# Kernel optimization log

Hardware: AMD Instinct MI355X
Metric: run time of the kernel (lower is better)

Reference implementation:

```python
import jax, jax.numpy as jnp
import numpy as np
from jax import lax

D_MODEL = 1024
D_STATE = 16
D_CONV = 4
EXPAND = 2
D_INNER = EXPAND * D_MODEL          # 2048
DT_RANK = (D_MODEL + 15) // 16      # 64


def setup_inputs() -> dict:
    key = jax.random.key(0)
    ks = jax.random.split(key, 12)
    B, L = 2, 2048
    s = lambda *sh: 1.0 / np.sqrt(sh[-1])
    inp = {
        "x": jax.random.normal(ks[0], (B, L, D_MODEL), jnp.float32),
        "in_proj_w": jax.random.normal(ks[1], (2 * D_INNER, D_MODEL), jnp.float32) * s(0, D_MODEL),
        "conv_w": jax.random.normal(ks[2], (D_INNER, 1, D_CONV), jnp.float32) * s(0, D_CONV),
        "conv_b": jax.random.normal(ks[3], (D_INNER,), jnp.float32) * 0.01,
        "x_proj_w": jax.random.normal(ks[4], (DT_RANK + 2 * D_STATE, D_INNER), jnp.float32) * s(0, D_INNER),
        "dt_proj_w": jax.random.normal(ks[5], (D_INNER, DT_RANK), jnp.float32) * s(0, DT_RANK),
        "dt_proj_b": jax.random.normal(ks[6], (D_INNER,), jnp.float32) * 0.1 - 4.0,  # softplus(dt) small
        "A_log": jnp.log(jnp.broadcast_to(jnp.arange(1, D_STATE + 1, dtype=jnp.float32), (D_INNER, D_STATE))),
        "D": jnp.ones((D_INNER,), jnp.float32),
        "out_proj_w": jax.random.normal(ks[7], (D_MODEL, D_INNER), jnp.float32) * s(0, D_INNER),
        "ln_w": jnp.ones((D_MODEL,), jnp.float32),
        "ln_b": jnp.zeros((D_MODEL,), jnp.float32),
    }
    return inp


def _mamba(x, in_proj_w, conv_w, conv_b, x_proj_w, dt_proj_w, dt_proj_b, A_log, D, out_proj_w):
    B, L, _ = x.shape
    xz = jnp.einsum("bld,ed->ble", x, in_proj_w)          # [B,L,2*d_inner]
    xi, z = jnp.split(xz, 2, axis=-1)                       # each [B,L,d_inner]

    # causal depthwise conv1d over time
    xt = jnp.transpose(xi, (0, 2, 1))                       # [B,d_inner,L]
    xc = lax.conv_general_dilated(
        xt, conv_w, window_strides=(1,), padding=[(D_CONV - 1, 0)],
        dimension_numbers=("NCH", "OIH", "NCH"), feature_group_count=D_INNER)
    xc = jax.nn.silu(xc + conv_b[None, :, None])            # [B,d_inner,L]
    u = jnp.transpose(xc, (0, 2, 1))                        # [B,L,d_inner]

    x_dbl = jnp.einsum("bld,ed->ble", u, x_proj_w)          # [B,L,dt_rank+2N]
    dt, Bm, Cm = jnp.split(x_dbl, [DT_RANK, DT_RANK + D_STATE], axis=-1)
    delta = jax.nn.softplus(jnp.einsum("blr,dr->bld", dt, dt_proj_w) + dt_proj_b)  # [B,L,d_inner]

    A = -jnp.exp(A_log)                                     # [d_inner,N]

    def step(h, inputs):
        d_t, B_t, C_t, u_t = inputs                         # [B,d], [B,N], [B,N], [B,d]
        dA = jnp.exp(d_t[..., None] * A)                    # [B,d_inner,N]
        h = dA * h + (d_t * u_t)[..., None] * B_t[:, None, :]
        y_t = jnp.einsum("bdn,bn->bd", h, C_t)
        return h, y_t

    xs = (jnp.transpose(delta, (1, 0, 2)), jnp.transpose(Bm, (1, 0, 2)),
          jnp.transpose(Cm, (1, 0, 2)), jnp.transpose(u, (1, 0, 2)))
    h0 = jnp.zeros((B, D_INNER, D_STATE), x.dtype)
    _, ys = lax.scan(step, h0, xs)                          # ys [L,B,d_inner]
    y = jnp.transpose(ys, (1, 0, 2)) + u * D                # skip connection
    y = y * jax.nn.silu(z)                                  # gate
    return jnp.einsum("bld,ed->ble", y, out_proj_w)         # [B,L,d_model]


def reference(x, in_proj_w, conv_w, conv_b, x_proj_w, dt_proj_w, dt_proj_b,
              A_log, D, out_proj_w, ln_w, ln_b):
    residual = x
    y = _mamba(x, in_proj_w, conv_w, conv_b, x_proj_w, dt_proj_w, dt_proj_b,
               A_log, D, out_proj_w)
    # dropout is identity in eval; residual + LayerNorm
    h = y + residual
    mu = jnp.mean(h, axis=-1, keepdims=True)
    var = jnp.var(h, axis=-1, keepdims=True)
    return (h - mu) * lax.rsqrt(var + 1e-5) * ln_w + ln_b
```

## Files before the change

kernel.cpp:

```cpp
#include <hip/hip_runtime.h>

typedef unsigned short u16;
typedef __attribute__((ext_vector_type(8))) short bf8_t;
typedef __attribute__((ext_vector_type(4))) float f4_t;
typedef __attribute__((ext_vector_type(4))) unsigned short u16x4;
typedef __attribute__((ext_vector_type(8))) unsigned short u16x8;

__device__ __forceinline__ float b2f(u16 h) {
  union { unsigned u; float f; } v; v.u = ((unsigned)h) << 16; return v.f;
}
__device__ __forceinline__ u16 f2b(float f) {
  union { float f; unsigned u; } v; v.f = f;
  unsigned u = v.u;
  u += 0x7fffu + ((u >> 16) & 1u);
  return (u16)(u >> 16);
}

#define AS1C(p) ((const __attribute__((address_space(1))) void*)(p))
#define AS3(p)  ((__attribute__((address_space(3))) void*)(p))

__global__ __launch_bounds__(256)
void cvt_all(const float* __restrict__ x, const float* __restrict__ inW,
             const float* __restrict__ xprojW, const float* __restrict__ dtW,
             const float* __restrict__ outW,
             u16* __restrict__ xb, u16* __restrict__ inWb, u16* __restrict__ xpb,
             u16* __restrict__ dtWb, u16* __restrict__ outWb)
{
  int i = blockIdx.x * 256 + threadIdx.x;
  if (i >= 2703360) return;
  const float* s; u16* d; int off;
  if (i < 1048576)      { s = x;      d = xb;    off = i; }
  else if (i < 2097152) { s = inW;    d = inWb;  off = i - 1048576; }
  else if (i < 2146304) { s = xprojW; d = xpb;   off = i - 2097152; }
  else if (i < 2179072) { s = dtW;    d = dtWb;  off = i - 2146304; }
  else                  { s = outW;   d = outWb; off = i - 2179072; }
  f4_t v = *(const f4_t*)(s + (size_t)off * 4);
  u16x4 o;
#pragma unroll
  for (int j = 0; j < 4; ++j) o[j] = f2b(v[j]);
  *(u16x4*)(d + (size_t)off * 4) = o;
}

__device__ __forceinline__ void stage64(const u16* g, int ld, int row0, int rowmax,
                                        int k0, u16* lds, int wid, int lane) {
  int qg = (lane & 7) ^ ((lane >> 3) & 7);
#pragma unroll
  for (int c = 0; c < 4; ++c) {
    int chunk = wid * 4 + c;
    int r = row0 + chunk * 8 + (lane >> 3);
    if (r > rowmax) r = rowmax;
    const u16* gp = g + (size_t)r * ld + k0 + qg * 8;
    __builtin_amdgcn_global_load_lds(AS1C(gp), AS3(lds + chunk * 512), 16, 0, 0);
  }
}

template<int EPI>
__device__ __forceinline__ void gemm_body(const u16* __restrict__ A, int lda,
             const u16* __restrict__ Bt, int ldb,
             int Kblk, int Nact,
             u16* __restrict__ o16, float* __restrict__ of32,
             const float* __restrict__ biasf)
{
  __shared__ u16 lsA[128 * 64];
  __shared__ u16 lsB[128 * 64];
  const int tid = threadIdx.x;
  const int wid = tid >> 6, lane = tid & 63;
  const int wm = wid >> 1, wn = wid & 1;
  const int lrow = lane & 15;
  const int kq = lane >> 4;
  const int sw = lrow & 7;
  const int m0 = blockIdx.y * 128;
  const int n0 = (EPI == 1) ? 0 : blockIdx.x * 128;
  int kbase = 0;
  if (EPI == 1) kbase = blockIdx.x * Kblk;

  f4_t acc[4][4];
#pragma unroll
  for (int i = 0; i < 4; ++i)
#pragma unroll
    for (int j = 0; j < 4; ++j) acc[i][j] = {0.f, 0.f, 0.f, 0.f};

  for (int kt = kbase; kt < kbase + Kblk; kt += 64) {
    stage64(A,  lda, m0, 0x3fffffff, kt, lsA, wid, lane);
    stage64(Bt, ldb, n0, Nact - 1,   kt, lsB, wid, lane);
    __syncthreads();
#pragma unroll
    for (int h = 0; h < 2; ++h) {
      const int lk = ((h * 4 + kq) ^ sw) * 8;
      bf8_t af[4], bfr[4];
#pragma unroll
      for (int mi = 0; mi < 4; ++mi)
        af[mi] = *(const bf8_t*)&lsA[(wm * 64 + mi * 16 + lrow) * 64 + lk];
#pragma unroll
      for (int ni = 0; ni < 4; ++ni)
        bfr[ni] = *(const bf8_t*)&lsB[(wn * 64 + ni * 16 + lrow) * 64 + lk];
#pragma unroll
      for (int mi = 0; mi < 4; ++mi)
#pragma unroll
        for (int ni = 0; ni < 4; ++ni)
          acc[mi][ni] = __builtin_amdgcn_mfma_f32_16x16x32_bf16(af[mi], bfr[ni], acc[mi][ni], 0, 0, 0);
    }
    __syncthreads();
  }

  const int rq = (lane >> 4) * 4;
#pragma unroll
  for (int mi = 0; mi < 4; ++mi) {
#pragma unroll
    for (int ni = 0; ni < 4; ++ni) {
#pragma unroll
      for (int r = 0; r < 4; ++r) {
        int m = m0 + wm * 64 + mi * 16 + rq + r;
        int n = n0 + wn * 64 + ni * 16 + lrow;
        float v = acc[mi][ni][r];
        if (EPI == 1) {
          if (n < 96) of32[((size_t)blockIdx.x * 4096 + m) * 96 + n] = v;
        } else if (EPI == 2) {
          float t = v + biasf[n];
          float sp = (t > 20.f) ? t : log1pf(__expf(t));
          o16[(size_t)m * 2048 + n] = f2b(sp);
        }
      }
    }
  }
}

__global__ __launch_bounds__(256)
void gemm_xp(const u16* A, int lda, const u16* Bt, int ldb, int Kblk, int Nact,
             u16* o16, float* of32, const float* biasf)
{ gemm_body<1>(A, lda, Bt, ldb, Kblk, Nact, o16, of32, biasf); }

__global__ __launch_bounds__(256)
void gemm_dt(const u16* A, int lda, const u16* Bt, int ldb, int Kblk, int Nact,
             u16* o16, float* of32, const float* biasf)
{ gemm_body<2>(A, lda, Bt, ldb, Kblk, Nact, o16, of32, biasf); }


__device__ __forceinline__ void stageu(const u16* __restrict__ g, int ld,
                                       int row0, int k0, u16* ldsu,
                                       int wid, int lane) {
  int qg = (lane & 7) ^ ((lane >> 3) & 7);
#pragma unroll
  for (int j = 0; j < 2; ++j) {
    int rr = j * 64 + wid * 8 + (lane >> 3);
    const u16* gp = g + (size_t)(row0 + rr) * ld + k0 + qg * 8;
    __builtin_amdgcn_global_load_lds(AS1C(gp), AS3(ldsu + (j * 512 + wid * 64) * 8), 16, 0, 0);
  }
}

#define G8_BAR()   __builtin_amdgcn_s_barrier()
#define G8_LGKM0() do { asm volatile("s_waitcnt lgkmcnt(0)" ::: "memory"); \
                        __builtin_amdgcn_sched_barrier(0); } while (0)
#define G8_LGKM8() asm volatile("s_waitcnt lgkmcnt(8)" ::: "memory")
#define G8_VM(N)   do { asm volatile("s_waitcnt vmcnt(" #N ")" ::: "memory"); \
                        __builtin_amdgcn_sched_barrier(0); } while (0)

#define RD_A(base, MH) do { \
  _Pragma("unroll") \
  for (int mi_ = 0; mi_ < 4; ++mi_) { \
    af[mi_][0] = *(const bf8_t*)((base) + arow + ((MH) * 64 + mi_ * 16) * 64 + aq0); \
    af[mi_][1] = *(const bf8_t*)((base) + arow + ((MH) * 64 + mi_ * 16) * 64 + aq1); \
  } } while (0)

#define RD_B(base, NH) do { \
  _Pragma("unroll") \
  for (int ni_ = 0; ni_ < 2; ++ni_) { \
    bfr[NH][ni_][0] = *(const bf8_t*)((base) + brow + ((NH) * 32 + ni_ * 16) * 64 + aq0); \
    bfr[NH][ni_][1] = *(const bf8_t*)((base) + brow + ((NH) * 32 + ni_ * 16) * 64 + aq1); \
  } } while (0)

#define MMA(MH, NH) do { \
  __builtin_amdgcn_s_setprio(1); \
  _Pragma("unroll") \
  for (int mi_ = 0; mi_ < 4; ++mi_) \
    _Pragma("unroll") \
    for (int ni_ = 0; ni_ < 2; ++ni_) { \
      acc[(MH) * 4 + mi_][(NH) * 2 + ni_] = __builtin_amdgcn_mfma_f32_16x16x32_bf16( \
          af[mi_][0], bfr[NH][ni_][0], acc[(MH) * 4 + mi_][(NH) * 2 + ni_], 0, 0, 0); \
      acc[(MH) * 4 + mi_][(NH) * 2 + ni_] = __builtin_amdgcn_mfma_f32_16x16x32_bf16( \
          af[mi_][1], bfr[NH][ni_][1], acc[(MH) * 4 + mi_][(NH) * 2 + ni_], 0, 0, 0); \
    } \
  __builtin_amdgcn_s_setprio(0); \
} while (0)

__global__ __launch_bounds__(512, 2)
void gemm8_in(const u16* __restrict__ A, const u16* __restrict__ Bt,
              u16* __restrict__ o16)
{
  __shared__ u16 ls[65536];
  const int tid = threadIdx.x;
  const int wid = tid >> 6, lane = tid & 63;
  const int wm = wid >> 2, wn = wid & 3;
  const int lrow = lane & 15;
  const int kq = lane >> 4;
  const int sw = lrow & 7;
  const int m0 = blockIdx.y * 256;
  const int n0 = blockIdx.x * 256;
  u16* lsA0 = ls;
  u16* lsB0 = ls + 16384;
  u16* lsA1 = ls + 32768;
  u16* lsB1 = ls + 49152;
  const int arow = (wm * 128 + lrow) * 64;
  const int brow = (wn * 64 + lrow) * 64;
  const int aq0 = (kq ^ sw) * 8;
  const int aq1 = ((4 + kq) ^ sw) * 8;

  f4_t acc[8][4];
#pragma unroll
  for (int i = 0; i < 8; ++i)
#pragma unroll
    for (int j = 0; j < 4; ++j) acc[i][j] = {0.f, 0.f, 0.f, 0.f};
  bf8_t af[4][2];
  bf8_t bfr[2][2][2];

  stageu(A,  1024, m0,        0, lsA0,        wid, lane);
  stageu(A,  1024, m0 + 128,  0, lsA0 + 8192, wid, lane);
  stageu(Bt, 1024, n0,        0, lsB0,        wid, lane);
  stageu(Bt, 1024, n0 + 128,  0, lsB0 + 8192, wid, lane);
  stageu(Bt, 1024, n0,       64, lsB1,        wid, lane);
  stageu(Bt, 1024, n0 + 128, 64, lsB1 + 8192, wid, lane);
  G8_VM(4); G8_BAR();

#pragma unroll 1
  for (int i = 0; i < 7; ++i) {
    const int k1 = (2 * i + 1) * 64, k2 = k1 + 64, k3 = k1 + 128;
    RD_A(lsA0, 0); RD_B(lsB0, 0);
    stageu(A, 1024, m0, k1, lsA1, wid, lane);
    G8_LGKM8(); G8_BAR(); G8_LGKM0(); MMA(0, 0); G8_BAR();
    RD_B(lsB0, 1);
    stageu(A, 1024, m0 + 128, k1, lsA1 + 8192, wid, lane);
    G8_BAR(); G8_LGKM0(); MMA(0, 1); G8_BAR();
    RD_A(lsA0, 1);
    stageu(Bt, 1024, n0, k2, lsB0, wid, lane);
    G8_BAR(); G8_LGKM0(); MMA(1, 0); G8_BAR();
    stageu(Bt, 1024, n0 + 128, k2, lsB0 + 8192, wid, lane);
    G8_BAR(); G8_LGKM0(); MMA(1, 1); G8_VM(4); G8_BAR();
    RD_A(lsA1, 0); RD_B(lsB1, 0);
    stageu(A, 1024, m0, k2, lsA0, wid, lane);
    G8_LGKM8(); G8_BAR(); G8_LGKM0(); MMA(0, 0); G8_BAR();
    RD_B(lsB1, 1);
    stageu(A, 1024, m0 + 128, k2, lsA0 + 8192, wid, lane);
    G8_BAR(); G8_LGKM0(); MMA(0, 1); G8_BAR();
    RD_A(lsA1, 1);
    stageu(Bt, 1024, n0, k3, lsB1, wid, lane);
    G8_BAR(); G8_LGKM0(); MMA(1, 0); G8_BAR();
    stageu(Bt, 1024, n0 + 128, k3, lsB1 + 8192, wid, lane);
    G8_BAR(); G8_LGKM0(); MMA(1, 1); G8_VM(4); G8_BAR();
  }

  {
    const int k1 = 960;
    RD_A(lsA0, 0); RD_B(lsB0, 0);
    stageu(A, 1024, m0, k1, lsA1, wid, lane);
    G8_LGKM8(); G8_BAR(); G8_LGKM0(); MMA(0, 0); G8_BAR();
    RD_B(lsB0, 1);
    stageu(A, 1024, m0 + 128, k1, lsA1 + 8192, wid, lane);
    G8_BAR(); G8_LGKM0(); MMA(0, 1); G8_BAR();
    RD_A(lsA0, 1);
    G8_BAR(); G8_LGKM0(); MMA(1, 0); G8_BAR();
    G8_BAR(); G8_LGKM0(); MMA(1, 1); G8_VM(0); G8_BAR();
    RD_A(lsA1, 0); RD_B(lsB1, 0);
    G8_BAR(); G8_LGKM0(); MMA(0, 0); G8_BAR();
    RD_B(lsB1, 1);
    G8_BAR(); G8_LGKM0(); MMA(0, 1); G8_BAR();
    RD_A(lsA1, 1);
    G8_BAR(); G8_LGKM0(); MMA(1, 0); G8_BAR();
    G8_LGKM0(); MMA(1, 1);
  }

  const int rq = (lane >> 4) * 4;
#pragma unroll
  for (int mi = 0; mi < 8; ++mi) {
#pragma unroll
    for (int ni = 0; ni < 4; ++ni) {
#pragma unroll
      for (int r = 0; r < 4; ++r) {
        int m = m0 + wm * 128 + mi * 16 + rq + r;
        int n = n0 + wn * 64 + ni * 16 + lrow;
        float v = acc[mi][ni][r];
        if (n < 2048) o16[(size_t)m * 2048 + n] = f2b(v);
        else          o16[(size_t)8388608 + (size_t)m * 2048 + (n - 2048)] = f2b(v);
      }
    }
  }
}


#define O4_RD_A(base, KH) do { \
  _Pragma("unroll") \
  for (int mi_ = 0; mi_ < 4; ++mi_) \
    af4[mi_][KH] = *(const bf8_t*)((base) + arow + mi_ * 1024 + ((KH) ? aq1 : aq0)); \
  } while (0)

#define O4_RD_B(base) do { \
  _Pragma("unroll") \
  for (int ni_ = 0; ni_ < 2; ++ni_) { \
    bf4[ni_][0] = *(const bf8_t*)((base) + brow + ni_ * 1024 + aq0); \
    bf4[ni_][1] = *(const bf8_t*)((base) + brow + ni_ * 1024 + aq1); \
  } } while (0)

#define O4_MMA(KH) do { \
  __builtin_amdgcn_s_setprio(1); \
  _Pragma("unroll") \
  for (int mi_ = 0; mi_ < 4; ++mi_) \
    _Pragma("unroll") \
    for (int ni_ = 0; ni_ < 2; ++ni_) \
      acc[mi_][ni_] = __builtin_amdgcn_mfma_f32_16x16x32_bf16( \
          af4[mi_][KH], bf4[ni_][KH], acc[mi_][ni_], 0, 0, 0); \
  __builtin_amdgcn_s_setprio(0); \
} while (0)

__global__ __launch_bounds__(512, 2)
void gemm4_out(const u16* __restrict__ A, const u16* __restrict__ Bt,
               const float* __restrict__ xres, float* __restrict__ yout)
{
  __shared__ u16 ls[32768];
  const int tid = threadIdx.x;
  const int wid = tid >> 6, lane = tid & 63;
  const int wm = wid >> 2, wn = wid & 3;
  const int lrow = lane & 15;
  const int kq = lane >> 4;
  const int sw = lrow & 7;
  const int m0 = blockIdx.y * 128;
  const int n0 = blockIdx.x * 128;
  u16* lsA0 = ls;
  u16* lsB0 = ls + 8192;
  u16* lsA1 = ls + 16384;
  u16* lsB1 = ls + 24576;
  const int arow = (wm * 64 + lrow) * 64;
  const int brow = (wn * 32 + lrow) * 64;
  const int aq0 = (kq ^ sw) * 8;
  const int aq1 = ((4 + kq) ^ sw) * 8;

  f4_t acc[4][2];
#pragma unroll
  for (int i = 0; i < 4; ++i)
#pragma unroll
    for (int j = 0; j < 2; ++j) acc[i][j] = {0.f, 0.f, 0.f, 0.f};
  bf8_t af4[4][2];
  bf8_t bf4[2][2];

  stageu(A,  2048, m0,  0, lsA0, wid, lane);
  stageu(Bt, 2048, n0,  0, lsB0, wid, lane);
  stageu(Bt, 2048, n0, 64, lsB1, wid, lane);
  G8_VM(2); G8_BAR();

#pragma unroll 1
  for (int i = 0; i < 15; ++i) {
    const int ka1 = (2 * i + 1) * 64;
    const int k2  = ka1 + 64;
    const int kb3 = ka1 + 128;
    O4_RD_A(lsA0, 0); O4_RD_B(lsB0);
    stageu(A, 2048, m0, ka1, lsA1, wid, lane);
    G8_BAR(); G8_LGKM0(); O4_MMA(0); G8_BAR();
    O4_RD_A(lsA0, 1);
    stageu(Bt, 2048, n0, k2, lsB0, wid, lane);
    G8_LGKM0(); O4_MMA(1); G8_VM(2); G8_BAR();
    O4_RD_A(lsA1, 0); O4_RD_B(lsB1);
    stageu(A, 2048, m0, k2, lsA0, wid, lane);
    G8_BAR(); G8_LGKM0(); O4_MMA(0); G8_BAR();
    O4_RD_A(lsA1, 1);
    stageu(Bt, 2048, n0, kb3, lsB1, wid, lane);
    G8_LGKM0(); O4_MMA(1); G8_VM(2); G8_BAR();
  }

  {
    O4_RD_A(lsA0, 0); O4_RD_B(lsB0);
    stageu(A, 2048, m0, 1984, lsA1, wid, lane);
    G8_BAR(); G8_LGKM0(); O4_MMA(0); G8_BAR();
    O4_RD_A(lsA0, 1);
    G8_LGKM0(); O4_MMA(1); G8_VM(0); G8_BAR();
    O4_RD_A(lsA1, 0); O4_RD_B(lsB1);
    G8_LGKM0(); O4_MMA(0);
    O4_RD_A(lsA1, 1);
    G8_LGKM0(); O4_MMA(1);
  }

  const int rq = (lane >> 4) * 4;
#pragma unroll
  for (int mi = 0; mi < 4; ++mi) {
#pragma unroll
    for (int ni = 0; ni < 2; ++ni) {
#pragma unroll
      for (int r = 0; r < 4; ++r) {
        int m = m0 + wm * 64 + mi * 16 + rq + r;
        int n = n0 + wn * 32 + ni * 16 + lrow;
        yout[(size_t)m * 1024 + n] = acc[mi][ni][r] + xres[(size_t)m * 1024 + n];
      }
    }
  }
}

__global__ __launch_bounds__(256)
void xproj_reduce(const float* __restrict__ part, u16* __restrict__ dtA,
                  float* __restrict__ bc)
{
  int idx = blockIdx.x * 256 + threadIdx.x;
  int m = idx / 96, n = idx - m * 96;
  float s = 0.f;
#pragma unroll
  for (int p = 0; p < 8; ++p) s += part[(size_t)p * 393216 + idx];
  if (n < 64) dtA[(size_t)m * 64 + n] = f2b(s);
  else        bc[(size_t)m * 32 + (n - 64)] = s;
}

__global__ __launch_bounds__(256)
void conv_silu(const u16* __restrict__ xib, const float* __restrict__ cw,
               const float* __restrict__ cb, u16* __restrict__ ub)
{
  int i = blockIdx.x * 256 + threadIdx.x;
  int c8 = (i & 255) * 8;
  int row = i >> 8;
  int l = row & 2047;
  const u16* base = xib + (size_t)row * 2048 + c8;
  u16x8 x0 = {0,0,0,0,0,0,0,0}, x1 = x0, x2 = x0, x3;
  x3 = *(const u16x8*)(base);
  if (l >= 1) x2 = *(const u16x8*)(base - 2048);
  if (l >= 2) x1 = *(const u16x8*)(base - 2 * 2048);
  if (l >= 3) x0 = *(const u16x8*)(base - 3 * 2048);
  f4_t cb0 = *(const f4_t*)(cb + c8);
  f4_t cb1 = *(const f4_t*)(cb + c8 + 4);
  u16x8 o;
#pragma unroll
  for (int j = 0; j < 8; ++j) {
    f4_t w = *(const f4_t*)(cw + (size_t)(c8 + j) * 4);
    float a = (j < 4 ? cb0[j] : cb1[j - 4])
            + w[0] * b2f(x0[j]) + w[1] * b2f(x1[j])
            + w[2] * b2f(x2[j]) + w[3] * b2f(x3[j]);
    float s = a / (1.f + __expf(-a));
    o[j] = f2b(s);
  }
  *(u16x8*)(ub + (size_t)row * 2048 + c8) = o;
}

__global__ __launch_bounds__(256)
void scan_s1(const u16* __restrict__ delta_bf, const u16* __restrict__ ub,
             const float* __restrict__ bc, const float* __restrict__ alog,
             u16* __restrict__ S, u16* __restrict__ Q)
{
  int blk = blockIdx.x;
  int g = blk & 7, c = (blk >> 3) & 63, b = blk >> 9;
  int d = g * 256 + threadIdx.x;
  float Av[16];
#pragma unroll
  for (int nq = 0; nq < 4; ++nq) {
    f4_t al = *(const f4_t*)(alog + (size_t)d * 16 + nq * 4);
#pragma unroll
    for (int j = 0; j < 4; ++j) Av[nq * 4 + j] = -__expf(al[j]);
  }
  float Av0 = Av[0];
  bool st = true;
#pragma unroll
  for (int n = 1; n < 16; ++n)
    st = st && (fabsf(Av[n] - (float)(n + 1) * Av0) <= 1e-3f * (float)(n + 1));
  f4_t Qr[4];
#pragma unroll
  for (int nq = 0; nq < 4; ++nq) Qr[nq] = {0.f,0.f,0.f,0.f};
  float Sd = 0.f;
  int row0 = b * 2048 + c * 32;
  if (st) {
#pragma unroll 2
    for (int i = 0; i < 32; ++i) {
      size_t row = (size_t)(row0 + i);
      float dlt = b2f(delta_bf[row * 2048 + d]);
      float uv  = b2f(ub[row * 2048 + d]);
      const float* bp = bc + row * 32;
      f4_t Bv[4];
#pragma unroll
      for (int nq = 0; nq < 4; ++nq) Bv[nq] = *(const f4_t*)(bp + nq * 4);
      float du = dlt * uv;
      float e1 = __expf(dlt * Av0);
      float a = e1;
      Sd += dlt;
#pragma unroll
      for (int n = 0; n < 16; ++n) {
        Qr[n >> 2][n & 3] = a * Qr[n >> 2][n & 3] + du * Bv[n >> 2][n & 3];
        a *= e1;
      }
    }
  } else {
#pragma unroll 2
    for (int i = 0; i < 32; ++i) {
      size_t row = (size_t)(row0 + i);
      float dlt = b2f(delta_bf[row * 2048 + d]);
      float uv  = b2f(ub[row * 2048 + d]);
      const float* bp = bc + row * 32;
      f4_t Bv[4];
#pragma unroll
      for (int nq = 0; nq < 4; ++nq) Bv[nq] = *(const f4_t*)(bp + nq * 4);
      float du = dlt * uv;
      Sd += dlt;
#pragma unroll
      for (int n = 0; n < 16; ++n) {
        float a = __expf(dlt * Av[n]);
        Qr[n >> 2][n & 3] = a * Qr[n >> 2][n & 3] + du * Bv[n >> 2][n & 3];
      }
    }
  }
  S[(size_t)(b * 64 + c) * 2048 + d] = f2b(Sd);
  size_t o = ((size_t)((b * 64 + c) * 2048 + d)) * 16;
  u16x8 q0, q1;
#pragma unroll
  for (int j = 0; j < 8; ++j) { q0[j] = f2b(Qr[j >> 2][j & 3]); q1[j] = f2b(Qr[(j + 8) >> 2][j & 3]); }
  *(u16x8*)(Q + o)     = q0;
  *(u16x8*)(Q + o + 8) = q1;
}

__global__ __launch_bounds__(256)
void scan_comb(const u16* __restrict__ S16, u16* __restrict__ Q,
               const float* __restrict__ alog)
{
  int idx = blockIdx.x * 256 + threadIdx.x;
  int b = idx >> 15, dn = idx & 32767;
  int d = dn >> 4;
  float Av = -__expf(alog[dn]);
  size_t qbase = (size_t)b * 2097152 + dn;
  size_t sbase = (size_t)b * 131072 + d;
  float H = 0.f;
#pragma unroll
  for (int cg = 0; cg < 4; ++cg) {
    float sv[16], qv[16];
#pragma unroll
    for (int j = 0; j < 16; ++j) {
      int c = cg * 16 + j;
      qv[j] = b2f(Q[qbase + (size_t)c * 32768]);
      sv[j] = b2f(S16[sbase + (size_t)c * 2048]);
    }
#pragma unroll
    for (int j = 0; j < 16; ++j) {
      int c = cg * 16 + j;
      Q[qbase + (size_t)c * 32768] = f2b(H);
      H = __expf(Av * sv[j]) * H + qv[j];
    }
  }
}

__global__ __launch_bounds__(256)
void scan_s3(const u16* __restrict__ delta_bf, const u16* __restrict__ ub,
             const float* __restrict__ bc, const float* __restrict__ alog,
             const u16* __restrict__ Q, const float* __restrict__ Dw,
             u16* __restrict__ zy)
{
  int blk = blockIdx.x;
  int g = blk & 7, c = (blk >> 3) & 63, b = blk >> 9;
  int d = g * 256 + threadIdx.x;
  float Av[16];
#pragma unroll
  for (int nq = 0; nq < 4; ++nq) {
    f4_t al = *(const f4_t*)(alog + (size_t)d * 16 + nq * 4);
#pragma unroll
    for (int j = 0; j < 4; ++j) Av[nq * 4 + j] = -__expf(al[j]);
  }
  float Av0 = Av[0];
  bool st = true;
#pragma unroll
  for (int n = 1; n < 16; ++n)
    st = st && (fabsf(Av[n] - (float)(n + 1) * Av0) <= 1e-3f * (float)(n + 1));
  f4_t h4[4];
  size_t o = ((size_t)((b * 64 + c) * 2048 + d)) * 16;
  {
    u16x8 q0 = *(const u16x8*)(Q + o);
    u16x8 q1 = *(const u16x8*)(Q + o + 8);
#pragma unroll
    for (int j = 0; j < 8; ++j) { h4[j >> 2][j & 3] = b2f(q0[j]); h4[(j + 8) >> 2][j & 3] = b2f(q1[j]); }
  }
  float Dv = Dw[d];
  int row0 = b * 2048 + c * 32;
  if (st) {
#pragma unroll 2
    for (int i = 0; i < 32; ++i) {
      size_t row = (size_t)(row0 + i);
      float dlt = b2f(delta_bf[row * 2048 + d]);
      float uv  = b2f(ub[row * 2048 + d]);
      const float* bp = bc + row * 32;
      f4_t Bv[4], Cv[4];
#pragma unroll
      for (int nq = 0; nq < 4; ++nq) { Bv[nq] = *(const f4_t*)(bp + nq * 4); Cv[nq] = *(const f4_t*)(bp + 16 + nq * 4); }
      float du = dlt * uv;
      float e1 = __expf(dlt * Av0);
      float a = e1;
      float y = 0.f;
#pragma unroll
      for (int n = 0; n < 16; ++n) {
        float hn = a * h4[n >> 2][n & 3] + du * Bv[n >> 2][n & 3];
        h4[n >> 2][n & 3] = hn;
        y += hn * Cv[n >> 2][n & 3];
        a *= e1;
      }
      float zv = b2f(zy[row * 2048 + d]);
      float ov = (y + Dv * uv) * (zv / (1.f + __expf(-zv)));
      zy[row * 2048 + d] = f2b(ov);
    }
  } else {
#pragma unroll 2
    for (int i = 0; i < 32; ++i) {
      size_t row = (size_t)(row0 + i);
      float dlt = b2f(delta_bf[row * 2048 + d]);
      float uv  = b2f(ub[row * 2048 + d]);
      const float* bp = bc + row * 32;
      f4_t Bv[4], Cv[4];
#pragma unroll
      for (int nq = 0; nq < 4; ++nq) { Bv[nq] = *(const f4_t*)(bp + nq * 4); Cv[nq] = *(const f4_t*)(bp + 16 + nq * 4); }
      float du = dlt * uv;
      float y = 0.f;
#pragma unroll
      for (int n = 0; n < 16; ++n) {
        float a = __expf(dlt * Av[n]);
        float hn = a * h4[n >> 2][n & 3] + du * Bv[n >> 2][n & 3];
        h4[n >> 2][n & 3] = hn;
        y += hn * Cv[n >> 2][n & 3];
      }
      float zv = b2f(zy[row * 2048 + d]);
      float ov = (y + Dv * uv) * (zv / (1.f + __expf(-zv)));
      zy[row * 2048 + d] = f2b(ov);
    }
  }
}

__global__ __launch_bounds__(256)
void ln_kernel(const float* __restrict__ hv,
               const float* __restrict__ lnw, const float* __restrict__ lnb,
               float* __restrict__ outp)
{
  __shared__ float ssum[4], ssq[4];
  int row = blockIdx.x, t = threadIdx.x;
  f4_t v4 = *(const f4_t*)(hv + (size_t)row * 1024 + t * 4);
  float v[4], s = 0.f, q = 0.f;
#pragma unroll
  for (int j = 0; j < 4; ++j) { v[j] = v4[j]; s += v[j]; q += v[j] * v[j]; }
#pragma unroll
  for (int m = 32; m; m >>= 1) { s += __shfl_xor(s, m, 64); q += __shfl_xor(q, m, 64); }
  int wv = t >> 6;
  if ((t & 63) == 0) { ssum[wv] = s; ssq[wv] = q; }
  __syncthreads();
  s = ssum[0] + ssum[1] + ssum[2] + ssum[3];
  q = ssq[0] + ssq[1] + ssq[2] + ssq[3];
  float mu = s * (1.f / 1024.f);
  float var = q * (1.f / 1024.f) - mu * mu;
  float rs = rsqrtf(var + 1e-5f);
  f4_t o;
#pragma unroll
  for (int j = 0; j < 4; ++j)
    o[j] = (v[j] - mu) * rs * lnw[t * 4 + j] + lnb[t * 4 + j];
  *(f4_t*)(outp + (size_t)row * 1024 + t * 4) = o;
}

extern "C" void kernel_launch(void* const* d_in, const int* in_sizes, int n_in,
                              void* d_out, int out_size, void* d_ws, size_t ws_size,
                              hipStream_t stream)
{
  const float* x      = (const float*)d_in[0];
  const float* inW    = (const float*)d_in[1];
  const float* convW  = (const float*)d_in[2];
  const float* convB  = (const float*)d_in[3];
  const float* xprojW = (const float*)d_in[4];
  const float* dtW    = (const float*)d_in[5];
  const float* dtB    = (const float*)d_in[6];
  const float* alog   = (const float*)d_in[7];
  const float* Dw     = (const float*)d_in[8];
  const float* outW   = (const float*)d_in[9];
  const float* lnw    = (const float*)d_in[10];
  const float* lnb    = (const float*)d_in[11];
  float* out = (float*)d_out;

  char* ws = (char*)d_ws;
  u16*   xiz    = (u16*)(ws);
  u16*   zy     = xiz + 8388608;
  u16*   xb     = (u16*)(ws + 33554432);
  u16*   inWb   = xb + 4194304;
  u16*   u_bf   = (u16*)(ws + 33554432);
  u16*   dtA    = (u16*)(ws + 50331648);
  float* bc     = (float*)(ws + 50855936);
  u16*   xprojWb= (u16*)(ws + 51380224);
  u16*   dtWb   = (u16*)(ws + 51773440);
  u16*   outWb  = (u16*)(ws + 52035584);
  u16*   delta  = xiz;
  float* xpart  = (float*)d_out;
  u16*   Sbuf   = dtA;
  u16*   Qbuf   = (u16*)d_out;
  float* yout   = (float*)d_out;

  dim3 blk(256);
  cvt_all<<<10560, blk, 0, stream>>>(x, inW, xprojW, dtW, outW,
                                     xb, inWb, xprojWb, dtWb, outWb);
  gemm8_in<<<dim3(16, 16), dim3(512), 0, stream>>>(xb, inWb, xiz);
  conv_silu<<<4096, blk, 0, stream>>>(xiz, convW, convB, u_bf);
  gemm_xp<<<dim3(8, 32), blk, 0, stream>>>(u_bf, 2048, xprojWb, 2048, 256, 96, nullptr, xpart, nullptr);
  xproj_reduce<<<1536, blk, 0, stream>>>(xpart, dtA, bc);
  gemm_dt<<<dim3(16, 32), blk, 0, stream>>>(dtA, 64, dtWb, 64, 64, 2048, delta, nullptr, dtB);
  scan_s1<<<1024, blk, 0, stream>>>(delta, u_bf, bc, alog, Sbuf, Qbuf);
  scan_comb<<<256, blk, 0, stream>>>(Sbuf, Qbuf, alog);
  scan_s3<<<1024, blk, 0, stream>>>(delta, u_bf, bc, alog, Qbuf, Dw, zy);
  gemm4_out<<<dim3(8, 32), dim3(512), 0, stream>>>(zy, outWb, x, yout);
  ln_kernel<<<4096, blk, 0, stream>>>(yout, lnw, lnb, out);
}
```

Before: 298.6 us.

## Use 4-wave 64x64 warp tiles in out-proj GEMM and bf16 x_proj partials

The out-projection GEMM drops from 8 waves to 4 waves per block, so each wave now computes a 64x64 tile instead of 64x32. That raises MFMA work per LDS read of A and lowers barrier participation, at the cost of more accumulator registers and fewer waves to hide latency. The x_proj split-K partial sums are also written as bf16 instead of fp32, halving partial traffic to the reduce kernel. This adds rounding error to dt, B and C before summation.

```diff
diff --git a/kernel.cpp b/kernel.cpp
--- a/kernel.cpp
+++ b/kernel.cpp
@@ -58,8 +58,7 @@
 __device__ __forceinline__ void gemm_body(const u16* __restrict__ A, int lda,
              const u16* __restrict__ Bt, int ldb,
              int Kblk, int Nact,
-             u16* __restrict__ o16, float* __restrict__ of32,
-             const float* __restrict__ biasf)
+             u16* __restrict__ o16, const float* __restrict__ biasf)
 {
   __shared__ u16 lsA[128 * 64];
   __shared__ u16 lsB[128 * 64];
@@ -114,7 +113,7 @@
         int n = n0 + wn * 64 + ni * 16 + lrow;
         float v = acc[mi][ni][r];
         if (EPI == 1) {
-          if (n < 96) of32[((size_t)blockIdx.x * 4096 + m) * 96 + n] = v;
+          if (n < 96) o16[((size_t)blockIdx.x * 4096 + m) * 96 + n] = f2b(v);
         } else if (EPI == 2) {
           float t = v + biasf[n];
           float sp = (t > 20.f) ? t : log1pf(__expf(t));
@@ -127,13 +126,13 @@
 
 __global__ __launch_bounds__(256)
 void gemm_xp(const u16* A, int lda, const u16* Bt, int ldb, int Kblk, int Nact,
-             u16* o16, float* of32, const float* biasf)
-{ gemm_body<1>(A, lda, Bt, ldb, Kblk, Nact, o16, of32, biasf); }
+             u16* o16, const float* biasf)
+{ gemm_body<1>(A, lda, Bt, ldb, Kblk, Nact, o16, biasf); }
 
 __global__ __launch_bounds__(256)
 void gemm_dt(const u16* A, int lda, const u16* Bt, int ldb, int Kblk, int Nact,
-             u16* o16, float* of32, const float* biasf)
-{ gemm_body<2>(A, lda, Bt, ldb, Kblk, Nact, o16, of32, biasf); }
+             u16* o16, const float* biasf)
+{ gemm_body<2>(A, lda, Bt, ldb, Kblk, Nact, o16, biasf); }
 
 
 __device__ __forceinline__ void stageu(const u16* __restrict__ g, int ld,
@@ -286,38 +285,38 @@
 }
 
 
-#define O4_RD_A(base, KH) do { \
+#define X4_RD_A(base, KH) do { \
   _Pragma("unroll") \
   for (int mi_ = 0; mi_ < 4; ++mi_) \
-    af4[mi_][KH] = *(const bf8_t*)((base) + arow + mi_ * 1024 + ((KH) ? aq1 : aq0)); \
+    afx[mi_] = *(const bf8_t*)((base) + (wm * 64 + mi_ * 16 + lrow) * 64 + ((KH) ? aq1 : aq0)); \
   } while (0)
 
-#define O4_RD_B(base) do { \
+#define X4_RD_B(base) do { \
   _Pragma("unroll") \
-  for (int ni_ = 0; ni_ < 2; ++ni_) { \
-    bf4[ni_][0] = *(const bf8_t*)((base) + brow + ni_ * 1024 + aq0); \
-    bf4[ni_][1] = *(const bf8_t*)((base) + brow + ni_ * 1024 + aq1); \
+  for (int ni_ = 0; ni_ < 4; ++ni_) { \
+    bfx[ni_][0] = *(const bf8_t*)((base) + (wn * 64 + ni_ * 16 + lrow) * 64 + aq0); \
+    bfx[ni_][1] = *(const bf8_t*)((base) + (wn * 64 + ni_ * 16 + lrow) * 64 + aq1); \
   } } while (0)
 
-#define O4_MMA(KH) do { \
+#define X4_MMA(KH) do { \
   __builtin_amdgcn_s_setprio(1); \
   _Pragma("unroll") \
   for (int mi_ = 0; mi_ < 4; ++mi_) \
     _Pragma("unroll") \
-    for (int ni_ = 0; ni_ < 2; ++ni_) \
+    for (int ni_ = 0; ni_ < 4; ++ni_) \
       acc[mi_][ni_] = __builtin_amdgcn_mfma_f32_16x16x32_bf16( \
-          af4[mi_][KH], bf4[ni_][KH], acc[mi_][ni_], 0, 0, 0); \
+          afx[mi_], bfx[ni_][KH], acc[mi_][ni_], 0, 0, 0); \
   __builtin_amdgcn_s_setprio(0); \
 } while (0)
 
-__global__ __launch_bounds__(512, 2)
+__global__ __launch_bounds__(256, 2)
 void gemm4_out(const u16* __restrict__ A, const u16* __restrict__ Bt,
                const float* __restrict__ xres, float* __restrict__ yout)
 {
   __shared__ u16 ls[32768];
   const int tid = threadIdx.x;
   const int wid = tid >> 6, lane = tid & 63;
-  const int wm = wid >> 2, wn = wid & 3;
+  const int wm = wid >> 1, wn = wid & 1;
   const int lrow = lane & 15;
   const int kq = lane >> 4;
   const int sw = lrow & 7;
@@ -327,64 +326,62 @@
   u16* lsB0 = ls + 8192;
   u16* lsA1 = ls + 16384;
   u16* lsB1 = ls + 24576;
-  const int arow = (wm * 64 + lrow) * 64;
-  const int brow = (wn * 32 + lrow) * 64;
   const int aq0 = (kq ^ sw) * 8;
   const int aq1 = ((4 + kq) ^ sw) * 8;
 
-  f4_t acc[4][2];
+  f4_t acc[4][4];
 #pragma unroll
   for (int i = 0; i < 4; ++i)
 #pragma unroll
-    for (int j = 0; j < 2; ++j) acc[i][j] = {0.f, 0.f, 0.f, 0.f};
-  bf8_t af4[4][2];
-  bf8_t bf4[2][2];
-
-  stageu(A,  2048, m0,  0, lsA0, wid, lane);
-  stageu(Bt, 2048, n0,  0, lsB0, wid, lane);
-  stageu(Bt, 2048, n0, 64, lsB1, wid, lane);
-  G8_VM(2); G8_BAR();
+    for (int j = 0; j < 4; ++j) acc[i][j] = {0.f, 0.f, 0.f, 0.f};
+  bf8_t afx[4];
+  bf8_t bfx[4][2];
+
+  stage64(A,  2048, m0, 0x3fffffff,  0, lsA0, wid, lane);
+  stage64(Bt, 2048, n0, 0x3fffffff,  0, lsB0, wid, lane);
+  stage64(Bt, 2048, n0, 0x3fffffff, 64, lsB1, wid, lane);
+  G8_VM(4); G8_BAR();
 
 #pragma unroll 1
   for (int i = 0; i < 15; ++i) {
     const int ka1 = (2 * i + 1) * 64;
     const int k2  = ka1 + 64;
     const int kb3 = ka1 + 128;
-    O4_RD_A(lsA0, 0); O4_RD_B(lsB0);
-    stageu(A, 2048, m0, ka1, lsA1, wid, lane);
-    G8_BAR(); G8_LGKM0(); O4_MMA(0); G8_BAR();
-    O4_RD_A(lsA0, 1);
-    stageu(Bt, 2048, n0, k2, lsB0, wid, lane);
-    G8_LGKM0(); O4_MMA(1); G8_VM(2); G8_BAR();
-    O4_RD_A(lsA1, 0); O4_RD_B(lsB1);
-    stageu(A, 2048, m0, k2, lsA0, wid, lane);
-    G8_BAR(); G8_LGKM0(); O4_MMA(0); G8_BAR();
-    O4_RD_A(lsA1, 1);
-    stageu(Bt, 2048, n0, kb3, lsB1, wid, lane);
-    G8_LGKM0(); O4_MMA(1); G8_VM(2); G8_BAR();
+    X4_RD_A(lsA0, 0); X4_RD_B(lsB0);
+    stage64(A, 2048, m0, 0x3fffffff, ka1, lsA1, wid, lane);
+    G8_BAR(); G8_LGKM0(); X4_MMA(0); G8_BAR();
+    X4_RD_A(lsA0, 1);
+    stage64(Bt, 2048, n0, 0x3fffffff, k2, lsB0, wid, lane);
+    G8_LGKM0(); X4_MMA(1); G8_VM(4); G8_BAR();
+    X4_RD_A(lsA1, 0); X4_RD_B(lsB1);
+    stage64(A, 2048, m0, 0x3fffffff, k2, lsA0, wid, lane);
+    G8_BAR(); G8_LGKM0(); X4_MMA(0); G8_BAR();
+    X4_RD_A(lsA1, 1);
+    stage64(Bt, 2048, n0, 0x3fffffff, kb3, lsB1, wid, lane);
+    G8_LGKM0(); X4_MMA(1); G8_VM(4); G8_BAR();
   }
 
   {
-    O4_RD_A(lsA0, 0); O4_RD_B(lsB0);
-    stageu(A, 2048, m0, 1984, lsA1, wid, lane);
-    G8_BAR(); G8_LGKM0(); O4_MMA(0); G8_BAR();
-    O4_RD_A(lsA0, 1);
-    G8_LGKM0(); O4_MMA(1); G8_VM(0); G8_BAR();
-    O4_RD_A(lsA1, 0); O4_RD_B(lsB1);
-    G8_LGKM0(); O4_MMA(0);
-    O4_RD_A(lsA1, 1);
-    G8_LGKM0(); O4_MMA(1);
+    X4_RD_A(lsA0, 0); X4_RD_B(lsB0);
+    stage64(A, 2048, m0, 0x3fffffff, 1984, lsA1, wid, lane);
+    G8_BAR(); G8_LGKM0(); X4_MMA(0); G8_BAR();
+    X4_RD_A(lsA0, 1);
+    G8_LGKM0(); X4_MMA(1); G8_VM(0); G8_BAR();
+    X4_RD_A(lsA1, 0); X4_RD_B(lsB1);
+    G8_LGKM0(); X4_MMA(0);
+    X4_RD_A(lsA1, 1);
+    G8_LGKM0(); X4_MMA(1);
   }
 
   const int rq = (lane >> 4) * 4;
 #pragma unroll
   for (int mi = 0; mi < 4; ++mi) {
 #pragma unroll
-    for (int ni = 0; ni < 2; ++ni) {
+    for (int ni = 0; ni < 4; ++ni) {
 #pragma unroll
       for (int r = 0; r < 4; ++r) {
         int m = m0 + wm * 64 + mi * 16 + rq + r;
-        int n = n0 + wn * 32 + ni * 16 + lrow;
+        int n = n0 + wn * 64 + ni * 16 + lrow;
         yout[(size_t)m * 1024 + n] = acc[mi][ni][r] + xres[(size_t)m * 1024 + n];
       }
     }
@@ -392,14 +389,14 @@
 }
 
 __global__ __launch_bounds__(256)
-void xproj_reduce(const float* __restrict__ part, u16* __restrict__ dtA,
+void xproj_reduce(const u16* __restrict__ part, u16* __restrict__ dtA,
                   float* __restrict__ bc)
 {
   int idx = blockIdx.x * 256 + threadIdx.x;
   int m = idx / 96, n = idx - m * 96;
   float s = 0.f;
 #pragma unroll
-  for (int p = 0; p < 8; ++p) s += part[(size_t)p * 393216 + idx];
+  for (int p = 0; p < 8; ++p) s += b2f(part[(size_t)p * 393216 + idx]);
   if (n < 64) dtA[(size_t)m * 64 + n] = f2b(s);
   else        bc[(size_t)m * 32 + (n - 64)] = s;
 }
@@ -675,7 +672,7 @@
   u16*   dtWb   = (u16*)(ws + 51773440);
   u16*   outWb  = (u16*)(ws + 52035584);
   u16*   delta  = xiz;
-  float* xpart  = (float*)d_out;
+  u16*   xpart  = (u16*)d_out;
   u16*   Sbuf   = dtA;
   u16*   Qbuf   = (u16*)d_out;
   float* yout   = (float*)d_out;
@@ -685,12 +682,12 @@
                                      xb, inWb, xprojWb, dtWb, outWb);
   gemm8_in<<<dim3(16, 16), dim3(512), 0, stream>>>(xb, inWb, xiz);
   conv_silu<<<4096, blk, 0, stream>>>(xiz, convW, convB, u_bf);
-  gemm_xp<<<dim3(8, 32), blk, 0, stream>>>(u_bf, 2048, xprojWb, 2048, 256, 96, nullptr, xpart, nullptr);
+  gemm_xp<<<dim3(8, 32), blk, 0, stream>>>(u_bf, 2048, xprojWb, 2048, 256, 96, xpart, nullptr);
   xproj_reduce<<<1536, blk, 0, stream>>>(xpart, dtA, bc);
-  gemm_dt<<<dim3(16, 32), blk, 0, stream>>>(dtA, 64, dtWb, 64, 64, 2048, delta, nullptr, dtB);
+  gemm_dt<<<dim3(16, 32), blk, 0, stream>>>(dtA, 64, dtWb, 64, 64, 2048, delta, dtB);
   scan_s1<<<1024, blk, 0, stream>>>(delta, u_bf, bc, alog, Sbuf, Qbuf);
   scan_comb<<<256, blk, 0, stream>>>(Sbuf, Qbuf, alog);
   scan_s3<<<1024, blk, 0, stream>>>(delta, u_bf, bc, alog, Qbuf, Dw, zy);
-  gemm4_out<<<dim3(8, 32), dim3(512), 0, stream>>>(zy, outWb, x, yout);
+  gemm4_out<<<dim3(8, 32), blk, 0, stream>>>(zy, outWb, x, yout);
   ln_kernel<<<4096, blk, 0, stream>>>(yout, lnw, lnb, out);
 }
```

New measurement: 297.5 us. About the same (-0.4%).
